# Optimization experiments

Hardware: AMD Instinct MI355X
Metric: run time of the kernel (lower is better)

## Reference

```python
import jax, jax.numpy as jnp
import numpy as np

LOG1000 = 6.9077542789816375  # ln(1000)


def setup_inputs() -> dict:
    key = jax.random.key(0)
    kx, kp = jax.random.split(key)
    x = jax.random.normal(kx, (65536, 128), dtype=jnp.float32)
    points = jax.random.normal(kp, (2048, 128), dtype=jnp.float32)
    beta_raw = jnp.array([-3.5], dtype=jnp.float32)
    return {"x": x, "points": points, "beta_raw": beta_raw}


def reference(x, points, beta_raw):
    t1 = jnp.sum(x * x, axis=-1, keepdims=True)            # [N, 1]
    t2 = jnp.sum(points * points, axis=-1)[None, :]        # [1, P]
    t3 = 2.0 * jnp.einsum('nd,pd->np', x, points)          # [N, P]
    d2 = jnp.clip(t1 + t2 - t3, 0.0)
    min_d = jnp.min(d2, axis=-1)                           # [N]
    # translated sigmoid
    beta = jax.nn.softplus(beta_raw)                       # [1]
    alpha = -beta * LOG1000
    return jax.nn.sigmoid((min_d + alpha) / beta)
```

## Files before the change

### kernel.cpp

```cpp
#include <hip/hip_runtime.h>


#define NROWS 65536
#define NPTS  2048
#define DIMS  128
#define LOG1000F 6.9077542789816375f
#define STAGE_PTS 256
#define NSTAGES (NPTS / STAGE_PTS)

typedef __attribute__((ext_vector_type(8))) int i32x8;
typedef __attribute__((ext_vector_type(4))) float f32x4;

union AFrag { int d[8]; i32x8 v; };
union BFrag { uint4 u4[2]; i32x8 v; };

__global__ __launch_bounds__(256) void prep_points_kernel(
    const float* __restrict__ pts, unsigned char* __restrict__ ptsf8,
    float* __restrict__ pnorm)
{
    int tid  = threadIdx.x;
    int lane = tid & 63;
    int w    = tid >> 6;
    int pt   = blockIdx.x * 4 + w;
    const float2 v = *reinterpret_cast<const float2*>(
        pts + (size_t)pt * DIMS + lane * 2);
    int pk = __builtin_amdgcn_cvt_pk_fp8_f32(v.x, v.y, 0, false);
    *reinterpret_cast<unsigned short*>(ptsf8 + (size_t)pt * DIMS + lane * 2) =
        (unsigned short)(pk & 0xFFFF);
    float ss = v.x * v.x + v.y * v.y;
    ss += __shfl_xor(ss, 1, 64);
    ss += __shfl_xor(ss, 2, 64);
    ss += __shfl_xor(ss, 4, 64);
    ss += __shfl_xor(ss, 8, 64);
    ss += __shfl_xor(ss, 16, 64);
    ss += __shfl_xor(ss, 32, 64);
    if (lane == 0) pnorm[pt] = ss;
}

__global__ __launch_bounds__(256, 2) void distnet_main_kernel(
    const float* __restrict__ x, const unsigned char* __restrict__ ptsf8,
    const float* __restrict__ pnorm, const float* __restrict__ beta_raw,
    float* __restrict__ out)
{
    __shared__ uint4 s_b[2][STAGE_PTS * DIMS / 16];
    __shared__ float s_pn[NPTS];
    __shared__ float s_xn[128];

    int tid  = threadIdx.x;
    for (int i = tid; i < NPTS / 4; i += 256)
        *reinterpret_cast<float4*>(&s_pn[i * 4]) =
            reinterpret_cast<const float4*>(pnorm)[i];

    int wave = tid >> 6;
    int lane = tid & 63;
    int m    = lane & 15;
    int q    = lane >> 4;
    int r0   = blockIdx.x * 128 + wave * 32;

    AFrag afrag[2];
#pragma unroll
    for (int t = 0; t < 2; ++t) {
        const float* xp = x + (size_t)(r0 + t * 16 + m) * DIMS + q * 32;
        float ss = 0.f;
#pragma unroll
        for (int d = 0; d < 8; ++d) {
            float4 v = *reinterpret_cast<const float4*>(xp + d * 4);
            int w0 = __builtin_amdgcn_cvt_pk_fp8_f32(v.x, v.y, 0, false);
            w0 = __builtin_amdgcn_cvt_pk_fp8_f32(v.z, v.w, w0, true);
            afrag[t].d[d] = w0;
            ss += v.x * v.x + v.y * v.y + v.z * v.z + v.w * v.w;
        }
        ss += __shfl_xor(ss, 16, 64);
        ss += __shfl_xor(ss, 32, 64);
        if (lane < 16) s_xn[wave * 32 + t * 16 + lane] = ss;
    }

    const unsigned char* gbase = ptsf8;
    auto issue_stage = [&](int s, int buf) {
#pragma unroll
        for (int i = 0; i < 8; ++i) {
            int tt = wave * 4 + (i >> 1);
            int c  = i & 1;
            size_t pbyte = (size_t)(s * STAGE_PTS + tt * 16 + m) * DIMS
                           + (size_t)q * 32 + (size_t)c * 16;
            const void* g = gbase + pbyte;
            void* l = (void*)&s_b[buf][(tt * 2 + c) * 64];
            __builtin_amdgcn_global_load_lds(
                (const __attribute__((address_space(1))) unsigned int*)g,
                (__attribute__((address_space(3))) unsigned int*)l,
                16, 0, 0);
        }
    };

    issue_stage(0, 0);

    float runmin[2][4] = {{1e30f, 1e30f, 1e30f, 1e30f},
                          {1e30f, 1e30f, 1e30f, 1e30f}};

    for (int s = 0; s < NSTAGES; ++s) {
        __syncthreads();
        if (s + 1 < NSTAGES) issue_stage(s + 1, (s + 1) & 1);

        const uint4* bbuf = &s_b[s & 1][0];
#pragma unroll
        for (int t = 0; t < 16; ++t) {
            BFrag bf;
            bf.u4[0] = bbuf[(t * 2 + 0) * 64 + lane];
            bf.u4[1] = bbuf[(t * 2 + 1) * 64 + lane];
            float pn = s_pn[s * STAGE_PTS + t * 16 + m];
            f32x4 acc0 = {0.f, 0.f, 0.f, 0.f};
            f32x4 acc1 = {0.f, 0.f, 0.f, 0.f};
            acc0 = __builtin_amdgcn_mfma_scale_f32_16x16x128_f8f6f4(
                afrag[0].v, bf.v, acc0, 0, 0, 0, 0x7F7F7F7F, 0, 0x7F7F7F7F);
            acc1 = __builtin_amdgcn_mfma_scale_f32_16x16x128_f8f6f4(
                afrag[1].v, bf.v, acc1, 0, 0, 0, 0x7F7F7F7F, 0, 0x7F7F7F7F);
#pragma unroll
            for (int r = 0; r < 4; ++r) {
                runmin[0][r] = fminf(runmin[0][r], fmaf(-2.f, acc0[r], pn));
                runmin[1][r] = fminf(runmin[1][r], fmaf(-2.f, acc1[r], pn));
            }
        }
    }

    float br    = beta_raw[0];
    float beta  = log1pf(expf(br));
    float alpha = -beta * LOG1000F;
#pragma unroll
    for (int t = 0; t < 2; ++t) {
#pragma unroll
        for (int r = 0; r < 4; ++r) {
            float v = runmin[t][r];
            v = fminf(v, __shfl_xor(v, 1, 64));
            v = fminf(v, __shfl_xor(v, 2, 64));
            v = fminf(v, __shfl_xor(v, 4, 64));
            v = fminf(v, __shfl_xor(v, 8, 64));
            if (m == 0) {
                float xnv = s_xn[wave * 32 + t * 16 + q * 4 + r];
                float d2  = fmaxf(xnv + v, 0.f);
                float z   = (d2 + alpha) / beta;
                out[r0 + t * 16 + q * 4 + r] = 1.f / (1.f + expf(-z));
            }
        }
    }
}

extern "C" void kernel_launch(void* const* d_in, const int* in_sizes, int n_in,
                              void* d_out, int out_size, void* d_ws, size_t ws_size,
                              hipStream_t stream) {
    const float* x        = (const float*)d_in[0];
    const float* pts      = (const float*)d_in[1];
    const float* beta_raw = (const float*)d_in[2];
    float* out            = (float*)d_out;

    unsigned char* ptsf8 = (unsigned char*)d_ws;
    float* pnorm = (float*)((char*)d_ws + (size_t)NPTS * DIMS);

    prep_points_kernel<<<NPTS / 4, 256, 0, stream>>>(pts, ptsf8, pnorm);
    distnet_main_kernel<<<NROWS / 128, 256, 0, stream>>>(x, ptsf8, pnorm,
                                                         beta_raw, out);
}
```

Measured before the change: 99.03 us.

## Split points across waves so each wave reuses all row fragments, drop per-stage barrier

Each wave now holds fp8 A fragments for all 128 rows of the block and processes only the point tiles it loaded itself, instead of 32 rows against every tile. This cuts LDS reads of point fragments by four per wave. Because each wave only reads data it fetched, the per-stage __syncthreads is replaced by a wave-local waitcnt. A shared-memory min reduction across the four waves is added at the end. The cost is higher register use for the larger A fragment and accumulator arrays, plus an extra barrier and reduction in the epilogue.

```diff
diff --git a/kernel.cpp b/kernel.cpp
--- a/kernel.cpp
+++ b/kernel.cpp
@@ -45,35 +45,14 @@
     __shared__ uint4 s_b[2][STAGE_PTS * DIMS / 16];
     __shared__ float s_pn[NPTS];
     __shared__ float s_xn[128];
+    __shared__ float s_part[4 * 128];
 
     int tid  = threadIdx.x;
-    for (int i = tid; i < NPTS / 4; i += 256)
-        *reinterpret_cast<float4*>(&s_pn[i * 4]) =
-            reinterpret_cast<const float4*>(pnorm)[i];
-
     int wave = tid >> 6;
     int lane = tid & 63;
     int m    = lane & 15;
     int q    = lane >> 4;
-    int r0   = blockIdx.x * 128 + wave * 32;
-
-    AFrag afrag[2];
-#pragma unroll
-    for (int t = 0; t < 2; ++t) {
-        const float* xp = x + (size_t)(r0 + t * 16 + m) * DIMS + q * 32;
-        float ss = 0.f;
-#pragma unroll
-        for (int d = 0; d < 8; ++d) {
-            float4 v = *reinterpret_cast<const float4*>(xp + d * 4);
-            int w0 = __builtin_amdgcn_cvt_pk_fp8_f32(v.x, v.y, 0, false);
-            w0 = __builtin_amdgcn_cvt_pk_fp8_f32(v.z, v.w, w0, true);
-            afrag[t].d[d] = w0;
-            ss += v.x * v.x + v.y * v.y + v.z * v.z + v.w * v.w;
-        }
-        ss += __shfl_xor(ss, 16, 64);
-        ss += __shfl_xor(ss, 32, 64);
-        if (lane < 16) s_xn[wave * 32 + t * 16 + lane] = ss;
-    }
+    int r0   = blockIdx.x * 128;
 
     const unsigned char* gbase = ptsf8;
     auto issue_stage = [&](int s, int buf) {
@@ -94,39 +73,63 @@
 
     issue_stage(0, 0);
 
-    float runmin[2][4] = {{1e30f, 1e30f, 1e30f, 1e30f},
-                          {1e30f, 1e30f, 1e30f, 1e30f}};
+    for (int i = tid; i < NPTS / 4; i += 256)
+        *reinterpret_cast<float4*>(&s_pn[i * 4]) =
+            reinterpret_cast<const float4*>(pnorm)[i];
+
+    AFrag afrag[8];
+#pragma unroll
+    for (int t = 0; t < 8; ++t) {
+        const float* xp = x + (size_t)(r0 + t * 16 + m) * DIMS + q * 32;
+        float ss = 0.f;
+#pragma unroll
+        for (int d = 0; d < 8; ++d) {
+            float4 v = *reinterpret_cast<const float4*>(xp + d * 4);
+            int w0 = __builtin_amdgcn_cvt_pk_fp8_f32(v.x, v.y, 0, false);
+            w0 = __builtin_amdgcn_cvt_pk_fp8_f32(v.z, v.w, w0, true);
+            afrag[t].d[d] = w0;
+            ss += v.x * v.x + v.y * v.y + v.z * v.z + v.w * v.w;
+        }
+        ss += __shfl_xor(ss, 16, 64);
+        ss += __shfl_xor(ss, 32, 64);
+        if (wave == 0 && lane < 16) s_xn[t * 16 + lane] = ss;
+    }
+    __syncthreads();
+
+    float runmin[8][4];
+#pragma unroll
+    for (int t = 0; t < 8; ++t)
+#pragma unroll
+        for (int r = 0; r < 4; ++r) runmin[t][r] = 1e30f;
 
     for (int s = 0; s < NSTAGES; ++s) {
-        __syncthreads();
+        __builtin_amdgcn_s_waitcnt(0x0070);
         if (s + 1 < NSTAGES) issue_stage(s + 1, (s + 1) & 1);
 
         const uint4* bbuf = &s_b[s & 1][0];
 #pragma unroll
-        for (int t = 0; t < 16; ++t) {
+        for (int tl = 0; tl < 4; ++tl) {
+            int tt = wave * 4 + tl;
             BFrag bf;
-            bf.u4[0] = bbuf[(t * 2 + 0) * 64 + lane];
-            bf.u4[1] = bbuf[(t * 2 + 1) * 64 + lane];
-            float pn = s_pn[s * STAGE_PTS + t * 16 + m];
-            f32x4 acc0 = {0.f, 0.f, 0.f, 0.f};
-            f32x4 acc1 = {0.f, 0.f, 0.f, 0.f};
-            acc0 = __builtin_amdgcn_mfma_scale_f32_16x16x128_f8f6f4(
-                afrag[0].v, bf.v, acc0, 0, 0, 0, 0x7F7F7F7F, 0, 0x7F7F7F7F);
-            acc1 = __builtin_amdgcn_mfma_scale_f32_16x16x128_f8f6f4(
-                afrag[1].v, bf.v, acc1, 0, 0, 0, 0x7F7F7F7F, 0, 0x7F7F7F7F);
+            bf.u4[0] = bbuf[(tt * 2 + 0) * 64 + lane];
+            bf.u4[1] = bbuf[(tt * 2 + 1) * 64 + lane];
+            float pn = s_pn[s * STAGE_PTS + tt * 16 + m];
 #pragma unroll
-            for (int r = 0; r < 4; ++r) {
-                runmin[0][r] = fminf(runmin[0][r], fmaf(-2.f, acc0[r], pn));
-                runmin[1][r] = fminf(runmin[1][r], fmaf(-2.f, acc1[r], pn));
+            for (int t = 0; t < 8; ++t) {
+                f32x4 acc = {0.f, 0.f, 0.f, 0.f};
+                acc = __builtin_amdgcn_mfma_scale_f32_16x16x128_f8f6f4(
+                    afrag[t].v, bf.v, acc, 0, 0, 0,
+                    0x7F7F7F7F, 0, 0x7F7F7F7F);
+#pragma unroll
+                for (int r = 0; r < 4; ++r)
+                    runmin[t][r] = fminf(runmin[t][r],
+                                         fmaf(-2.f, acc[r], pn));
             }
         }
     }
 
-    float br    = beta_raw[0];
-    float beta  = log1pf(expf(br));
-    float alpha = -beta * LOG1000F;
 #pragma unroll
-    for (int t = 0; t < 2; ++t) {
+    for (int t = 0; t < 8; ++t) {
 #pragma unroll
         for (int r = 0; r < 4; ++r) {
             float v = runmin[t][r];
@@ -134,13 +137,21 @@
             v = fminf(v, __shfl_xor(v, 2, 64));
             v = fminf(v, __shfl_xor(v, 4, 64));
             v = fminf(v, __shfl_xor(v, 8, 64));
-            if (m == 0) {
-                float xnv = s_xn[wave * 32 + t * 16 + q * 4 + r];
-                float d2  = fmaxf(xnv + v, 0.f);
-                float z   = (d2 + alpha) / beta;
-                out[r0 + t * 16 + q * 4 + r] = 1.f / (1.f + expf(-z));
-            }
+            if (m == 0) s_part[wave * 128 + t * 16 + q * 4 + r] = v;
         }
+    }
+    __syncthreads();
+
+    if (tid < 128) {
+        float v = fminf(fminf(s_part[tid], s_part[128 + tid]),
+                        fminf(s_part[256 + tid], s_part[384 + tid]));
+        float xnv = s_xn[tid];
+        float d2  = fmaxf(xnv + v, 0.f);
+        float br    = beta_raw[0];
+        float beta  = log1pf(expf(br));
+        float alpha = -beta * LOG1000F;
+        float z = (d2 + alpha) / beta;
+        out[r0 + tid] = 1.f / (1.f + expf(-z));
     }
 }
 
```

Measured after the change: 115.8 us. 16.9% more time.
